# Kernel tuning notes

Measured on AMD Instinct MI355X. Metric: run time of the kernel, lower is better.

The kernel has to match this reference:

```python
import jax, jax.numpy as jnp
import numpy as np

N_NODES = 20000


def gcn_conv(x, src, dst, W, b, n):
    # PyG GCNConv: add self-loops, symmetric normalization, then aggregate.
    loop = jnp.arange(n, dtype=src.dtype)
    s = jnp.concatenate([src, loop])
    d = jnp.concatenate([dst, loop])
    w = jnp.ones(s.shape[0], dtype=x.dtype)
    deg = jax.ops.segment_sum(w, d, num_segments=n)  # in-degree at targets
    dinv = jnp.where(deg > 0, jax.lax.rsqrt(deg), 0.0)
    norm = dinv[s] * dinv[d]  # [E+n]
    h = x @ W  # [n, out]
    msg = h[s] * norm[:, None]  # gather + scale, [E+n, out]
    return jax.ops.segment_sum(msg, d, num_segments=n) + b


def gcn_stack(x, src, dst, W1, b1, W2, b2, n):
    h = jax.nn.relu(gcn_conv(x, src, dst, W1, b1, n))
    return gcn_conv(h, src, dst, W2, b2, n)


def setup_inputs() -> dict:
    key = jax.random.key(0)
    ks = jax.random.split(key, 12)
    n, e, din, dh, dout = N_NODES, 320000, 256, 256, 128
    x = jax.random.normal(ks[0], (n, din), dtype=jnp.float32)
    edge_index = jax.random.randint(ks[1], (2, e), 0, n, dtype=jnp.int64)
    g = lambda k, i, o: jax.random.normal(k, (i, o), dtype=jnp.float32) / np.sqrt(i)
    return {
        "x": x, "edge_index": edge_index,
        "Wf1": g(ks[2], din, dh), "bf1": jnp.zeros(dh, jnp.float32),
        "Wf2": g(ks[3], dh, dh), "bf2": jnp.zeros(dh, jnp.float32),
        "Wb1": g(ks[4], din, dh), "bb1": jnp.zeros(dh, jnp.float32),
        "Wb2": g(ks[5], dh, dh), "bb2": jnp.zeros(dh, jnp.float32),
        "Wfin": g(ks[6], 2 * dh, dout), "bfin": jnp.zeros(dout, jnp.float32),
    }


def reference(x, edge_index, Wf1, bf1, Wf2, bf2, Wb1, bb1, Wb2, bb2, Wfin, bfin):
    n = x.shape[0]
    src, dst = edge_index[0], edge_index[1]
    # forward-direction GCN stack
    x_fwd = gcn_stack(x, src, dst, Wf1, bf1, Wf2, bf2, n)
    # backward-direction GCN stack (edges reversed)
    x_bwd = gcn_stack(x, dst, src, Wb1, bb1, Wb2, bb2, n)
    x_combined = jnp.concatenate([x_fwd, x_bwd], axis=-1)  # [n, 2*hidden]
    return x_combined @ Wfin + bfin
```

## Files before the change

kernel.cpp:

```cpp
#include <hip/hip_runtime.h>

typedef unsigned int   u32;
typedef unsigned short u16;
typedef __attribute__((ext_vector_type(8))) short bf16x8;
typedef __attribute__((ext_vector_type(4))) float f32x4;

__device__ __forceinline__ u16 f2bf(float f) {
    u32 u = __float_as_uint(f);
    u32 r = u + 0x7fffu + ((u >> 16) & 1u);
    return (u16)(r >> 16);
}
__device__ __forceinline__ float bf2f(u16 h) {
    return __uint_as_float(((u32)h) << 16);
}
__device__ __forceinline__ float lof(u32 q) { return __uint_as_float(q << 16); }
__device__ __forceinline__ float hif(u32 q) { return __uint_as_float(q & 0xffff0000u); }
__device__ __forceinline__ u32 pk(float a, float b) {
    return (u32)f2bf(a) | ((u32)f2bf(b) << 16);
}
__device__ __forceinline__ void gl_lds16(const void* g, void* l) {
    __builtin_amdgcn_global_load_lds(
        (const __attribute__((address_space(1))) u32*)g,
        (__attribute__((address_space(3))) u32*)l, 16, 0, 0);
}
__device__ __forceinline__ void st16(void* dst, const u16* h) {
    uint4 q;
    q.x = (u32)h[0] | ((u32)h[1] << 16);
    q.y = (u32)h[2] | ((u32)h[3] << 16);
    q.z = (u32)h[4] | ((u32)h[5] << 16);
    q.w = (u32)h[6] | ((u32)h[7] << 16);
    *(uint4*)dst = q;
}

__global__ __launch_bounds__(256)
void k_deg(const int* __restrict__ src, const int* __restrict__ dst,
           int* __restrict__ deg_f, int* __restrict__ deg_b, int E) {
    int e = blockIdx.x * 256 + threadIdx.x;
    if (e < E) {
        atomicAdd(&deg_f[dst[e]], 1);
        atomicAdd(&deg_b[src[e]], 1);
    }
}

__global__ __launch_bounds__(256)
void k_scan1(const int* __restrict__ deg_f, const int* __restrict__ deg_b,
             float* __restrict__ dinv_f, float* __restrict__ dinv_b,
             int* __restrict__ bsum, int n, int nblk) {
    __shared__ int red[4];
    int dir = blockIdx.x >= nblk;
    int b = dir ? blockIdx.x - nblk : blockIdx.x;
    const int* deg = dir ? deg_b : deg_f;
    float* dinv = dir ? dinv_b : dinv_f;
    int idx = b * 256 + threadIdx.x;
    int d = 0;
    if (idx < n) {
        d = deg[idx];
        dinv[idx] = rsqrtf((float)(d + 1));
    }
    int s = d;
    s += __shfl_down(s, 32);
    s += __shfl_down(s, 16);
    s += __shfl_down(s, 8);
    s += __shfl_down(s, 4);
    s += __shfl_down(s, 2);
    s += __shfl_down(s, 1);
    int wv = threadIdx.x >> 6;
    if ((threadIdx.x & 63) == 0) red[wv] = s;
    __syncthreads();
    if (threadIdx.x == 0)
        bsum[blockIdx.x] = red[0] + red[1] + red[2] + red[3];
}

__global__ __launch_bounds__(256)
void k_scan2(const int* __restrict__ bsum, int* __restrict__ bpre, int nblk) {
    __shared__ int sm[256];
    int t = threadIdx.x;
    int seg = t >> 7;
    int i = t & 127;
    int val = (i < nblk) ? bsum[seg * nblk + i] : 0;
    sm[t] = val;
    __syncthreads();
    for (int s = 1; s < 128; s <<= 1) {
        int v = ((t & 127) >= s) ? sm[t - s] : 0;
        __syncthreads();
        sm[t] += v;
        __syncthreads();
    }
    if (i < nblk) bpre[seg * nblk + i] = sm[t] - val;
}

__global__ __launch_bounds__(256)
void k_scan3(const int* __restrict__ deg_f, const int* __restrict__ deg_b,
             const int* __restrict__ bpre,
             int* __restrict__ off_f, int* __restrict__ cur_f,
             int* __restrict__ off_b, int* __restrict__ cur_b,
             int n, int nblk, int E) {
    __shared__ int sm[256];
    int dir = blockIdx.x >= nblk;
    int b = dir ? blockIdx.x - nblk : blockIdx.x;
    const int* deg = dir ? deg_b : deg_f;
    int* off = dir ? off_b : off_f;
    int* cur = dir ? cur_b : cur_f;
    int base = bpre[blockIdx.x];
    int idx = b * 256 + threadIdx.x;
    int d = (idx < n) ? deg[idx] : 0;
    sm[threadIdx.x] = d;
    __syncthreads();
    for (int s = 1; s < 256; s <<= 1) {
        int v = (threadIdx.x >= s) ? sm[threadIdx.x - s] : 0;
        __syncthreads();
        sm[threadIdx.x] += v;
        __syncthreads();
    }
    if (idx < n) {
        int excl = base + sm[threadIdx.x] - d;
        off[idx] = excl;
        cur[idx] = excl;
    }
    if (blockIdx.x == 0 && threadIdx.x == 0) {
        off_f[n] = E;
        off_b[n] = E;
    }
}

__global__ __launch_bounds__(256)
void k_fill(const int* __restrict__ src, const int* __restrict__ dst,
            int* __restrict__ cur_f, int* __restrict__ cur_b,
            int* __restrict__ lst_f, int* __restrict__ lst_b, int E) {
    int e = blockIdx.x * 256 + threadIdx.x;
    if (e < E) {
        int s = src[e], d = dst[e];
        int pf = atomicAdd(&cur_f[d], 1);
        lst_f[pf] = s;
        int pb = atomicAdd(&cur_b[s], 1);
        lst_b[pb] = d;
    }
}

__global__ __launch_bounds__(256)
void k_wsplit5(const float* __restrict__ W0, const float* __restrict__ W1,
               const float* __restrict__ W2, const float* __restrict__ W3,
               const float* __restrict__ W4,
               u16* __restrict__ h0, u16* __restrict__ l0,
               u16* __restrict__ h1, u16* __restrict__ l1,
               u16* __restrict__ h2, u16* __restrict__ l2,
               u16* __restrict__ h3, u16* __restrict__ l3,
               u16* __restrict__ h4, u16* __restrict__ l4)
{
    int which = blockIdx.x >> 8;
    int sub = ((blockIdx.x & 255) << 8) | threadIdx.x;
    const float* W; u16 *H, *L; int kshift, N;
    switch (which) {
        case 0: W = W0; H = h0; L = l0; kshift = 8; N = 256; break;
        case 1: W = W1; H = h1; L = l1; kshift = 8; N = 256; break;
        case 2: W = W2; H = h2; L = l2; kshift = 8; N = 256; break;
        case 3: W = W3; H = h3; L = l3; kshift = 8; N = 256; break;
        default: W = W4; H = h4; L = l4; kshift = 9; N = 128; break;
    }
    int ni = sub >> kshift;
    int ki = sub & ((1 << kshift) - 1);
    float v = W[(size_t)ki * N + ni];
    u16 hh = f2bf(v);
    H[sub] = hh;
    L[sub] = f2bf(v - bf2f(hh));
}

__global__ __launch_bounds__(256)
void k_cvec(const float* __restrict__ bfin, const float* __restrict__ bf2,
            const float* __restrict__ bb2, const float* __restrict__ Wfin,
            float* __restrict__ cvec) {
    __shared__ float red[256];
    int j = blockIdx.x;
    int t = threadIdx.x;
    float s = bf2[t] * Wfin[(size_t)t * 128 + j]
            + bb2[t] * Wfin[(size_t)(t + 256) * 128 + j];
    red[t] = s;
    __syncthreads();
    for (int st = 128; st > 0; st >>= 1) {
        if (t < st) red[t] += red[t + st];
        __syncthreads();
    }
    if (t == 0) cvec[j] = red[0] + bfin[j];
}

template<int AMODE, int PASS3, int WLO>
__global__ __launch_bounds__(256)
void k_gemm2(const void* __restrict__ A0, const void* __restrict__ A1p,
             const u16* __restrict__ Alo0, const u16* __restrict__ Alo1,
             const u16* __restrict__ Bhi0, const u16* __restrict__ Blo0,
             const u16* __restrict__ Bhi1, const u16* __restrict__ Blo1, int ldb,
             u16* __restrict__ Chi0, u16* __restrict__ Clo0,
             u16* __restrict__ Chi1, u16* __restrict__ Clo1,
             const float* __restrict__ rs0, const float* __restrict__ rs1,
             int M, int N)
{
    constexpr int ALO = 8192;
    constexpr int BHI = PASS3 ? 16384 : 8192;
    constexpr int BLO = BHI + 8192;
    __shared__ char smem[PASS3 ? 32768 : 24576];

    const int z = blockIdx.z;
    const void* Aptr = z ? A1p : A0;
    const u16* Alo   = z ? Alo1 : Alo0;
    const u16* Bhi   = z ? Bhi1 : Bhi0;
    const u16* Blo   = z ? Blo1 : Blo0;
    u16* Chi         = z ? Chi1 : Chi0;
    u16* Clo         = z ? Clo1 : Clo0;
    const float* rowscale = z ? rs1 : rs0;

    const int tid  = threadIdx.x;
    const int lane = tid & 63;
    const int wid  = tid >> 6;
    const int wm   = wid >> 1, wn = wid & 1;
    const int bm   = blockIdx.x * 128;
    const int bn   = blockIdx.y * 128;

    f32x4 acc[4][4];
#pragma unroll
    for (int i = 0; i < 4; ++i)
#pragma unroll
        for (int j = 0; j < 4; ++j) acc[i][j] = (f32x4){0.f, 0.f, 0.f, 0.f};

    const int gsw  = ((lane >> 2) & 3) ^ ((lane >> 4) & 3);
    const int gsta = ((lane & 3) ^ gsw) << 4;
    const int sl   = (lane & 3) ^ ((lane >> 2) & 3);
    const int hi4  = lane >> 4;
    const int gsel = ((hi4 ^ sl) << 4);
    const int frow = lane & 15;

    for (int k0 = 0; k0 < 256; k0 += 32) {
        if (k0) __syncthreads();

#pragma unroll
        for (int p = 0; p < 2; ++p) {
            int c   = p * 4 + wid;
            int row = c * 16 + (lane >> 2);
            size_t rb = (size_t)(bn + row) * ldb + (size_t)k0 * 2 + gsta;
            gl_lds16((const char*)Bhi + rb, smem + BHI + c * 1024);
            gl_lds16((const char*)Blo + rb, smem + BLO + c * 1024);
        }
        if (AMODE == 0) {
            const u16* Ah = (const u16*)Aptr;
#pragma unroll
            for (int p = 0; p < 2; ++p) {
                int c   = p * 4 + wid;
                int row = c * 16 + (lane >> 2);
                int grow = bm + row; if (grow >= M) grow = M - 1;
                size_t rb = (size_t)grow * 512 + (size_t)k0 * 2 + gsta;
                gl_lds16((const char*)Ah + rb, smem + c * 1024);
                if (PASS3)
                    gl_lds16((const char*)Alo + rb, smem + ALO + c * 1024);
            }
        } else {
            const float* Af = (const float*)Aptr;
            int row  = tid >> 1;
            int half = tid & 1;
            int grow = bm + row; if (grow >= M) grow = M - 1;
            const float* srcp = Af + (size_t)grow * 256 + k0 + half * 16;
            float vv[16];
            *(float4*)(vv + 0)  = *(const float4*)(srcp + 0);
            *(float4*)(vv + 4)  = *(const float4*)(srcp + 4);
            *(float4*)(vv + 8)  = *(const float4*)(srcp + 8);
            *(float4*)(vv + 12) = *(const float4*)(srcp + 12);
            u16 h[16], l[16];
#pragma unroll
            for (int i = 0; i < 16; ++i) {
                h[i] = f2bf(vv[i]);
                l[i] = f2bf(vv[i] - bf2f(h[i]));
            }
            int swz = (row & 3) ^ ((row >> 2) & 3);
            char* dh = smem + row * 64;
            st16(dh + (((half * 2 + 0) ^ swz) << 4), h + 0);
            st16(dh + (((half * 2 + 1) ^ swz) << 4), h + 8);
            if (PASS3) {
                char* dl = smem + ALO + row * 64;
                st16(dl + (((half * 2 + 0) ^ swz) << 4), l + 0);
                st16(dl + (((half * 2 + 1) ^ swz) << 4), l + 8);
            }
        }
        __syncthreads();

        bf16x8 ah[4], al[4], bh[4], bl[4];
#pragma unroll
        for (int fm = 0; fm < 4; ++fm) {
            int r = wm * 64 + fm * 16 + frow;
            ah[fm] = *(const bf16x8*)(smem + r * 64 + gsel);
            if (PASS3) al[fm] = *(const bf16x8*)(smem + ALO + r * 64 + gsel);
        }
#pragma unroll
        for (int fn = 0; fn < 4; ++fn) {
            int r = wn * 64 + fn * 16 + frow;
            bh[fn] = *(const bf16x8*)(smem + BHI + r * 64 + gsel);
            bl[fn] = *(const bf16x8*)(smem + BLO + r * 64 + gsel);
        }
#pragma unroll
        for (int fm = 0; fm < 4; ++fm)
#pragma unroll
            for (int fn = 0; fn < 4; ++fn)
                acc[fm][fn] = __builtin_amdgcn_mfma_f32_16x16x32_bf16(ah[fm], bh[fn], acc[fm][fn], 0, 0, 0);
#pragma unroll
        for (int fm = 0; fm < 4; ++fm)
#pragma unroll
            for (int fn = 0; fn < 4; ++fn)
                acc[fm][fn] = __builtin_amdgcn_mfma_f32_16x16x32_bf16(ah[fm], bl[fn], acc[fm][fn], 0, 0, 0);
        if (PASS3) {
#pragma unroll
            for (int fm = 0; fm < 4; ++fm)
#pragma unroll
                for (int fn = 0; fn < 4; ++fn)
                    acc[fm][fn] = __builtin_amdgcn_mfma_f32_16x16x32_bf16(al[fm], bh[fn], acc[fm][fn], 0, 0, 0);
        }
    }

#pragma unroll
    for (int fm = 0; fm < 4; ++fm) {
#pragma unroll
        for (int q = 0; q < 4; ++q) {
            int row = bm + wm * 64 + fm * 16 + hi4 * 4 + q;
            if (row < M) {
                float s = rowscale ? rowscale[row] : 1.0f;
#pragma unroll
                for (int fn = 0; fn < 4; ++fn) {
                    int col = bn + wn * 64 + fn * 16 + frow;
                    float v = acc[fm][fn][q] * s;
                    u16 hb = f2bf(v);
                    Chi[(size_t)row * N + col] = hb;
                    if (WLO) Clo[(size_t)row * N + col] = f2bf(v - bf2f(hb));
                }
            }
        }
    }
}

__global__ __launch_bounds__(256)
void k_agg1(const u16* __restrict__ ghf, const u16* __restrict__ glf,
            const u16* __restrict__ ghb, const u16* __restrict__ glb,
            const int* __restrict__ off_f, const int* __restrict__ lst_f,
            const int* __restrict__ off_b, const int* __restrict__ lst_b,
            const float* __restrict__ dinv_f, const float* __restrict__ dinv_b,
            const float* __restrict__ b_f, const float* __restrict__ b_b,
            u16* __restrict__ ozf, u16* __restrict__ ozb, int n)
{
    int nb = gridDim.x >> 1;
    int stack = blockIdx.x >= nb;
    int bx = stack ? (blockIdx.x - nb) : blockIdx.x;
    const u16* gh = stack ? ghb : ghf;
    const u16* gl = stack ? glb : glf;
    const int* off = stack ? off_b : off_f;
    const int* lst = stack ? lst_b : lst_f;
    const float* dinv = stack ? dinv_b : dinv_f;
    const float* bias = stack ? b_b : b_f;
    u16* oz = stack ? ozb : ozf;

    int wv = threadIdx.x >> 6;
    int half = (threadIdx.x >> 5) & 1;
    int l = threadIdx.x & 31;
    int v = bx * 8 + wv * 2 + half;
    if (v >= n) return;
    int f0 = l * 8;

    uint4 qh = *(const uint4*)(gh + (size_t)v * 256 + f0);
    uint4 ql = *(const uint4*)(gl + (size_t)v * 256 + f0);
    float a0 = lof(qh.x) + lof(ql.x), a1 = hif(qh.x) + hif(ql.x);
    float a2 = lof(qh.y) + lof(ql.y), a3 = hif(qh.y) + hif(ql.y);
    float a4 = lof(qh.z) + lof(ql.z), a5 = hif(qh.z) + hif(ql.z);
    float a6 = lof(qh.w) + lof(ql.w), a7 = hif(qh.w) + hif(ql.w);

    int s0 = off[v], s1 = off[v + 1];
    int j = s0;
    for (; j + 4 <= s1; j += 4) {
        int u0 = lst[j], u1 = lst[j + 1], u2 = lst[j + 2], u3 = lst[j + 3];
        uint4 m0 = *(const uint4*)(gh + (size_t)u0 * 256 + f0);
        uint4 m1 = *(const uint4*)(gh + (size_t)u1 * 256 + f0);
        uint4 m2 = *(const uint4*)(gh + (size_t)u2 * 256 + f0);
        uint4 m3 = *(const uint4*)(gh + (size_t)u3 * 256 + f0);
        a0 += lof(m0.x) + lof(m1.x) + lof(m2.x) + lof(m3.x);
        a1 += hif(m0.x) + hif(m1.x) + hif(m2.x) + hif(m3.x);
        a2 += lof(m0.y) + lof(m1.y) + lof(m2.y) + lof(m3.y);
        a3 += hif(m0.y) + hif(m1.y) + hif(m2.y) + hif(m3.y);
        a4 += lof(m0.z) + lof(m1.z) + lof(m2.z) + lof(m3.z);
        a5 += hif(m0.z) + hif(m1.z) + hif(m2.z) + hif(m3.z);
        a6 += lof(m0.w) + lof(m1.w) + lof(m2.w) + lof(m3.w);
        a7 += hif(m0.w) + hif(m1.w) + hif(m2.w) + hif(m3.w);
    }
    for (; j < s1; ++j) {
        int u = lst[j];
        uint4 m = *(const uint4*)(gh + (size_t)u * 256 + f0);
        a0 += lof(m.x); a1 += hif(m.x);
        a2 += lof(m.y); a3 += hif(m.y);
        a4 += lof(m.z); a5 += hif(m.z);
        a6 += lof(m.w); a7 += hif(m.w);
    }
    float sc = dinv[v];
    float4 bA = *(const float4*)(bias + f0);
    float4 bB = *(const float4*)(bias + f0 + 4);
    float o0 = fmaxf(a0 * sc + bA.x, 0.f), o1 = fmaxf(a1 * sc + bA.y, 0.f);
    float o2 = fmaxf(a2 * sc + bA.z, 0.f), o3 = fmaxf(a3 * sc + bA.w, 0.f);
    float o4 = fmaxf(a4 * sc + bB.x, 0.f), o5 = fmaxf(a5 * sc + bB.y, 0.f);
    float o6 = fmaxf(a6 * sc + bB.z, 0.f), o7 = fmaxf(a7 * sc + bB.w, 0.f);
    uint4 r;
    r.x = pk(o0, o1); r.y = pk(o2, o3); r.z = pk(o4, o5); r.w = pk(o6, o7);
    *(uint4*)(oz + (size_t)v * 256 + f0) = r;
}

__global__ __launch_bounds__(256)
void k_agg2(const u16* __restrict__ yf, const u16* __restrict__ yb,
            const int* __restrict__ off_f, const int* __restrict__ lst_f,
            const int* __restrict__ off_b, const int* __restrict__ lst_b,
            const float* __restrict__ dinv_f, const float* __restrict__ dinv_b,
            const float* __restrict__ cvec, float* __restrict__ out, int n)
{
    int wv = threadIdx.x >> 6, lane = threadIdx.x & 63;
    int v = blockIdx.x * 4 + wv;
    if (v >= n) return;
    int dirb = lane >> 5;
    int l = lane & 31;
    int f0 = l * 4;

    const u16* y   = dirb ? yb : yf;
    const int* off = dirb ? off_b : off_f;
    const int* lst = dirb ? lst_b : lst_f;
    float dv = dirb ? dinv_b[v] : dinv_f[v];

    uint2 q = *(const uint2*)(y + (size_t)v * 128 + f0);
    float a0 = lof(q.x), a1 = hif(q.x), a2 = lof(q.y), a3 = hif(q.y);

    int s0 = off[v], s1 = off[v + 1];
    int j = s0;
    for (; j + 4 <= s1; j += 4) {
        int u0 = lst[j], u1 = lst[j + 1], u2 = lst[j + 2], u3 = lst[j + 3];
        uint2 m0 = *(const uint2*)(y + (size_t)u0 * 128 + f0);
        uint2 m1 = *(const uint2*)(y + (size_t)u1 * 128 + f0);
        uint2 m2 = *(const uint2*)(y + (size_t)u2 * 128 + f0);
        uint2 m3 = *(const uint2*)(y + (size_t)u3 * 128 + f0);
        a0 += lof(m0.x) + lof(m1.x) + lof(m2.x) + lof(m3.x);
        a1 += hif(m0.x) + hif(m1.x) + hif(m2.x) + hif(m3.x);
        a2 += lof(m0.y) + lof(m1.y) + lof(m2.y) + lof(m3.y);
        a3 += hif(m0.y) + hif(m1.y) + hif(m2.y) + hif(m3.y);
    }
    for (; j < s1; ++j) {
        int u = lst[j];
        uint2 m = *(const uint2*)(y + (size_t)u * 128 + f0);
        a0 += lof(m.x); a1 += hif(m.x);
        a2 += lof(m.y); a3 += hif(m.y);
    }
    float o0 = a0 * dv, o1 = a1 * dv, o2 = a2 * dv, o3 = a3 * dv;
    o0 += __shfl_xor(o0, 32);
    o1 += __shfl_xor(o1, 32);
    o2 += __shfl_xor(o2, 32);
    o3 += __shfl_xor(o3, 32);
    if (dirb == 0) {
        float4 c4 = *(const float4*)(cvec + f0);
        float4 o;
        o.x = o0 + c4.x; o.y = o1 + c4.y; o.z = o2 + c4.z; o.w = o3 + c4.w;
        *(float4*)(out + (size_t)v * 128 + f0) = o;
    }
}

extern "C" void kernel_launch(void* const* d_in, const int* in_sizes, int n_in,
                              void* d_out, int out_size, void* d_ws, size_t ws_size,
                              hipStream_t stream) {
    const float* x    = (const float*)d_in[0];
    const int*   ei   = (const int*)d_in[1];
    const float* Wf1  = (const float*)d_in[2];
    const float* bf1  = (const float*)d_in[3];
    const float* Wf2  = (const float*)d_in[4];
    const float* bf2  = (const float*)d_in[5];
    const float* Wb1  = (const float*)d_in[6];
    const float* bb1  = (const float*)d_in[7];
    const float* Wb2  = (const float*)d_in[8];
    const float* bb2  = (const float*)d_in[9];
    const float* Wfin = (const float*)d_in[10];
    const float* bfin = (const float*)d_in[11];
    float* out = (float*)d_out;

    const int n = in_sizes[0] / 256;
    const int E = in_sizes[1] / 2;
    const int* src = ei;
    const int* dst = ei + E;

    char* p = (char*)d_ws;
    auto take = [&](size_t bytes) -> void* {
        void* q = (void*)p;
        p += (bytes + 255) & ~(size_t)255;
        return q;
    };
    u16* P1f_h = (u16*)take((size_t)n * 256 * 2);
    u16* P1f_l = (u16*)take((size_t)n * 256 * 2);
    u16* P1b_h = (u16*)take((size_t)n * 256 * 2);
    u16* P1b_l = (u16*)take((size_t)n * 256 * 2);
    u16* Zf    = (u16*)take((size_t)n * 256 * 2);
    u16* Zb    = (u16*)take((size_t)n * 256 * 2);
    u16* H2f   = (u16*)take((size_t)n * 256 * 2);
    u16* H2b   = (u16*)take((size_t)n * 256 * 2);
    u16* Yf    = (u16*)take((size_t)n * 128 * 2);
    u16* Yb    = (u16*)take((size_t)n * 128 * 2);
    u16* w1f_h = (u16*)take(65536 * 2); u16* w1f_l = (u16*)take(65536 * 2);
    u16* w2f_h = (u16*)take(65536 * 2); u16* w2f_l = (u16*)take(65536 * 2);
    u16* w1b_h = (u16*)take(65536 * 2); u16* w1b_l = (u16*)take(65536 * 2);
    u16* w2b_h = (u16*)take(65536 * 2); u16* w2b_l = (u16*)take(65536 * 2);
    u16* wfin_h = (u16*)take(65536 * 2); u16* wfin_l = (u16*)take(65536 * 2);
    float* cvec = (float*)take(128 * sizeof(float));
    int*   deg_f  = (int*)take((size_t)n * sizeof(int));
    int*   deg_b  = (int*)take((size_t)n * sizeof(int));
    int*   off_f  = (int*)take((size_t)(n + 1) * sizeof(int));
    int*   off_b  = (int*)take((size_t)(n + 1) * sizeof(int));
    int*   cur_f  = (int*)take((size_t)n * sizeof(int));
    int*   cur_b  = (int*)take((size_t)n * sizeof(int));
    int*   lst_f  = (int*)take((size_t)E * sizeof(int));
    int*   lst_b  = (int*)take((size_t)E * sizeof(int));
    float* dinv_f = (float*)take((size_t)n * sizeof(float));
    float* dinv_b = (float*)take((size_t)n * sizeof(float));
    int*   bsum   = (int*)take(256 * sizeof(int));
    int*   bpre   = (int*)take(256 * sizeof(int));

    hipMemsetAsync(deg_f, 0, (size_t)n * sizeof(int), stream);
    hipMemsetAsync(deg_b, 0, (size_t)n * sizeof(int), stream);

    const int nblk = (n + 255) / 256;
    int eb = (E + 255) / 256;
    k_deg<<<eb, 256, 0, stream>>>(src, dst, deg_f, deg_b, E);
    k_scan1<<<2 * nblk, 256, 0, stream>>>(deg_f, deg_b, dinv_f, dinv_b, bsum, n, nblk);
    k_scan2<<<1, 256, 0, stream>>>(bsum, bpre, nblk);
    k_scan3<<<2 * nblk, 256, 0, stream>>>(deg_f, deg_b, bpre,
        off_f, cur_f, off_b, cur_b, n, nblk, E);
    k_fill<<<eb, 256, 0, stream>>>(src, dst, cur_f, cur_b, lst_f, lst_b, E);
    k_wsplit5<<<1280, 256, 0, stream>>>(Wf1, Wf2, Wb1, Wb2, Wfin,
        w1f_h, w1f_l, w2f_h, w2f_l, w1b_h, w1b_l, w2b_h, w2b_l, wfin_h, wfin_l);
    k_cvec<<<128, 256, 0, stream>>>(bfin, bf2, bb2, Wfin, cvec);

    const int gx = (n + 127) / 128;
    dim3 gBig(gx, 2, 2);
    dim3 gFin(gx, 1, 2);
    int ab = (n + 3) / 4;
    int a1b = 2 * ((n + 7) / 8);

    k_gemm2<1, 1, 1><<<gBig, 256, 0, stream>>>(x, x, nullptr, nullptr,
        w1f_h, w1f_l, w1b_h, w1b_l, 512,
        P1f_h, P1f_l, P1b_h, P1b_l, dinv_f, dinv_b, n, 256);
    k_agg1<<<a1b, 256, 0, stream>>>(P1f_h, P1f_l, P1b_h, P1b_l,
        off_f, lst_f, off_b, lst_b, dinv_f, dinv_b, bf1, bb1, Zf, Zb, n);
    k_gemm2<0, 0, 0><<<gBig, 256, 0, stream>>>(Zf, Zb, nullptr, nullptr,
        w2f_h, w2f_l, w2b_h, w2b_l, 512,
        H2f, nullptr, H2b, nullptr, dinv_f, dinv_b, n, 256);
    k_gemm2<0, 0, 0><<<gFin, 256, 0, stream>>>(H2f, H2b, nullptr, nullptr,
        wfin_h, wfin_l, wfin_h + 256, wfin_l + 256, 1024,
        Yf, nullptr, Yb, nullptr, nullptr, nullptr, n, 128);
    k_agg2<<<ab, 256, 0, stream>>>(Yf, Yb,
        off_f, lst_f, off_b, lst_b, dinv_f, dinv_b, cvec, out, n);
}
```

Baseline: 292.1 us.

## Drop split-bf16 low parts for x and layer-1 outputs, pre-convert x

Converts x to a single bf16 copy in a merged prep kernel, which also absorbs the weight-split and bias-vector kernels. The first GEMM then runs two MFMA passes instead of three and stores only a high bf16 output. The first aggregation reads one bf16 buffer instead of a hi/lo pair and gathers eight neighbours per iteration. This cuts memory traffic and MFMA work in the first layer at the cost of lower precision on the input and intermediate activations.

Measured after the change: 279.9 us. 1.04x faster.

```diff
diff --git a/kernel.cpp b/kernel.cpp
--- a/kernel.cpp
+++ b/kernel.cpp
@@ -22,14 +22,6 @@
     __builtin_amdgcn_global_load_lds(
         (const __attribute__((address_space(1))) u32*)g,
         (__attribute__((address_space(3))) u32*)l, 16, 0, 0);
-}
-__device__ __forceinline__ void st16(void* dst, const u16* h) {
-    uint4 q;
-    q.x = (u32)h[0] | ((u32)h[1] << 16);
-    q.y = (u32)h[2] | ((u32)h[3] << 16);
-    q.z = (u32)h[4] | ((u32)h[5] << 16);
-    q.w = (u32)h[6] | ((u32)h[7] << 16);
-    *(uint4*)dst = q;
 }
 
 __global__ __launch_bounds__(256)
@@ -138,74 +130,76 @@
 }
 
 __global__ __launch_bounds__(256)
-void k_wsplit5(const float* __restrict__ W0, const float* __restrict__ W1,
-               const float* __restrict__ W2, const float* __restrict__ W3,
-               const float* __restrict__ W4,
-               u16* __restrict__ h0, u16* __restrict__ l0,
-               u16* __restrict__ h1, u16* __restrict__ l1,
-               u16* __restrict__ h2, u16* __restrict__ l2,
-               u16* __restrict__ h3, u16* __restrict__ l3,
-               u16* __restrict__ h4, u16* __restrict__ l4)
+void k_prep(const float* __restrict__ W0, const float* __restrict__ W1,
+            const float* __restrict__ W2, const float* __restrict__ W3,
+            const float* __restrict__ W4,
+            u16* __restrict__ h0, u16* __restrict__ l0,
+            u16* __restrict__ h1, u16* __restrict__ l1,
+            u16* __restrict__ h2, u16* __restrict__ l2,
+            u16* __restrict__ h3, u16* __restrict__ l3,
+            u16* __restrict__ h4, u16* __restrict__ l4,
+            const float* __restrict__ bfin, const float* __restrict__ bf2,
+            const float* __restrict__ bb2, float* __restrict__ cvec,
+            const float* __restrict__ x, u16* __restrict__ xh, int xcount)
 {
-    int which = blockIdx.x >> 8;
-    int sub = ((blockIdx.x & 255) << 8) | threadIdx.x;
-    const float* W; u16 *H, *L; int kshift, N;
-    switch (which) {
-        case 0: W = W0; H = h0; L = l0; kshift = 8; N = 256; break;
-        case 1: W = W1; H = h1; L = l1; kshift = 8; N = 256; break;
-        case 2: W = W2; H = h2; L = l2; kshift = 8; N = 256; break;
-        case 3: W = W3; H = h3; L = l3; kshift = 8; N = 256; break;
-        default: W = W4; H = h4; L = l4; kshift = 9; N = 128; break;
-    }
-    int ni = sub >> kshift;
-    int ki = sub & ((1 << kshift) - 1);
-    float v = W[(size_t)ki * N + ni];
-    u16 hh = f2bf(v);
-    H[sub] = hh;
-    L[sub] = f2bf(v - bf2f(hh));
-}
-
-__global__ __launch_bounds__(256)
-void k_cvec(const float* __restrict__ bfin, const float* __restrict__ bf2,
-            const float* __restrict__ bb2, const float* __restrict__ Wfin,
-            float* __restrict__ cvec) {
     __shared__ float red[256];
-    int j = blockIdx.x;
+    int b = blockIdx.x;
     int t = threadIdx.x;
-    float s = bf2[t] * Wfin[(size_t)t * 128 + j]
-            + bb2[t] * Wfin[(size_t)(t + 256) * 128 + j];
-    red[t] = s;
-    __syncthreads();
-    for (int st = 128; st > 0; st >>= 1) {
-        if (t < st) red[t] += red[t + st];
+    if (b < 1280) {
+        int which = b >> 8;
+        int sub = ((b & 255) << 8) | t;
+        const float* W; u16 *H, *L; int kshift, N;
+        switch (which) {
+            case 0: W = W0; H = h0; L = l0; kshift = 8; N = 256; break;
+            case 1: W = W1; H = h1; L = l1; kshift = 8; N = 256; break;
+            case 2: W = W2; H = h2; L = l2; kshift = 8; N = 256; break;
+            case 3: W = W3; H = h3; L = l3; kshift = 8; N = 256; break;
+            default: W = W4; H = h4; L = l4; kshift = 9; N = 128; break;
+        }
+        int ni = sub >> kshift;
+        int ki = sub & ((1 << kshift) - 1);
+        float v = W[(size_t)ki * N + ni];
+        u16 hh = f2bf(v);
+        H[sub] = hh;
+        L[sub] = f2bf(v - bf2f(hh));
+    } else if (b < 1408) {
+        int j = b - 1280;
+        float s = bf2[t] * W4[(size_t)t * 128 + j]
+                + bb2[t] * W4[(size_t)(t + 256) * 128 + j];
+        red[t] = s;
         __syncthreads();
-    }
-    if (t == 0) cvec[j] = red[0] + bfin[j];
-}
-
-template<int AMODE, int PASS3, int WLO>
-__global__ __launch_bounds__(256)
-void k_gemm2(const void* __restrict__ A0, const void* __restrict__ A1p,
-             const u16* __restrict__ Alo0, const u16* __restrict__ Alo1,
-             const u16* __restrict__ Bhi0, const u16* __restrict__ Blo0,
-             const u16* __restrict__ Bhi1, const u16* __restrict__ Blo1, int ldb,
-             u16* __restrict__ Chi0, u16* __restrict__ Clo0,
-             u16* __restrict__ Chi1, u16* __restrict__ Clo1,
-             const float* __restrict__ rs0, const float* __restrict__ rs1,
-             int M, int N)
+        for (int st = 128; st > 0; st >>= 1) {
+            if (t < st) red[t] += red[t + st];
+            __syncthreads();
+        }
+        if (t == 0) cvec[j] = red[0] + bfin[j];
+    } else {
+        int i = (b - 1408) * 1024 + t * 4;
+        if (i < xcount) {
+            float4 v = *(const float4*)(x + i);
+            ushort4 h4v;
+            h4v.x = f2bf(v.x); h4v.y = f2bf(v.y);
+            h4v.z = f2bf(v.z); h4v.w = f2bf(v.w);
+            *(ushort4*)(xh + i) = h4v;
+        }
+    }
+}
+
+__global__ __launch_bounds__(256)
+void k_gemm(const u16* __restrict__ A0, const u16* __restrict__ A1p,
+            const u16* __restrict__ Bhi0, const u16* __restrict__ Blo0,
+            const u16* __restrict__ Bhi1, const u16* __restrict__ Blo1, int ldb,
+            u16* __restrict__ C0, u16* __restrict__ C1,
+            const float* __restrict__ rs0, const float* __restrict__ rs1,
+            int M, int N)
 {
-    constexpr int ALO = 8192;
-    constexpr int BHI = PASS3 ? 16384 : 8192;
-    constexpr int BLO = BHI + 8192;
-    __shared__ char smem[PASS3 ? 32768 : 24576];
+    __shared__ char smem[24576];
 
     const int z = blockIdx.z;
-    const void* Aptr = z ? A1p : A0;
-    const u16* Alo   = z ? Alo1 : Alo0;
-    const u16* Bhi   = z ? Bhi1 : Bhi0;
-    const u16* Blo   = z ? Blo1 : Blo0;
-    u16* Chi         = z ? Chi1 : Chi0;
-    u16* Clo         = z ? Clo1 : Clo0;
+    const u16* Ah  = z ? A1p : A0;
+    const u16* Bhi = z ? Bhi1 : Bhi0;
+    const u16* Blo = z ? Blo1 : Blo0;
+    u16* Chi       = z ? C1 : C0;
     const float* rowscale = z ? rs1 : rs0;
 
     const int tid  = threadIdx.x;
@@ -236,62 +230,30 @@
             int c   = p * 4 + wid;
             int row = c * 16 + (lane >> 2);
             size_t rb = (size_t)(bn + row) * ldb + (size_t)k0 * 2 + gsta;
-            gl_lds16((const char*)Bhi + rb, smem + BHI + c * 1024);
-            gl_lds16((const char*)Blo + rb, smem + BLO + c * 1024);
-        }
-        if (AMODE == 0) {
-            const u16* Ah = (const u16*)Aptr;
-#pragma unroll
-            for (int p = 0; p < 2; ++p) {
-                int c   = p * 4 + wid;
-                int row = c * 16 + (lane >> 2);
-                int grow = bm + row; if (grow >= M) grow = M - 1;
-                size_t rb = (size_t)grow * 512 + (size_t)k0 * 2 + gsta;
-                gl_lds16((const char*)Ah + rb, smem + c * 1024);
-                if (PASS3)
-                    gl_lds16((const char*)Alo + rb, smem + ALO + c * 1024);
-            }
-        } else {
-            const float* Af = (const float*)Aptr;
-            int row  = tid >> 1;
-            int half = tid & 1;
+            gl_lds16((const char*)Bhi + rb, smem + 8192 + c * 1024);
+            gl_lds16((const char*)Blo + rb, smem + 16384 + c * 1024);
+        }
+#pragma unroll
+        for (int p = 0; p < 2; ++p) {
+            int c   = p * 4 + wid;
+            int row = c * 16 + (lane >> 2);
             int grow = bm + row; if (grow >= M) grow = M - 1;
-            const float* srcp = Af + (size_t)grow * 256 + k0 + half * 16;
-            float vv[16];
-            *(float4*)(vv + 0)  = *(const float4*)(srcp + 0);
-            *(float4*)(vv + 4)  = *(const float4*)(srcp + 4);
-            *(float4*)(vv + 8)  = *(const float4*)(srcp + 8);
-            *(float4*)(vv + 12) = *(const float4*)(srcp + 12);
-            u16 h[16], l[16];
-#pragma unroll
-            for (int i = 0; i < 16; ++i) {
-                h[i] = f2bf(vv[i]);
-                l[i] = f2bf(vv[i] - bf2f(h[i]));
-            }
-            int swz = (row & 3) ^ ((row >> 2) & 3);
-            char* dh = smem + row * 64;
-            st16(dh + (((half * 2 + 0) ^ swz) << 4), h + 0);
-            st16(dh + (((half * 2 + 1) ^ swz) << 4), h + 8);
-            if (PASS3) {
-                char* dl = smem + ALO + row * 64;
-                st16(dl + (((half * 2 + 0) ^ swz) << 4), l + 0);
-                st16(dl + (((half * 2 + 1) ^ swz) << 4), l + 8);
-            }
+            size_t rb = (size_t)grow * 512 + (size_t)k0 * 2 + gsta;
+            gl_lds16((const char*)Ah + rb, smem + c * 1024);
         }
         __syncthreads();
 
-        bf16x8 ah[4], al[4], bh[4], bl[4];
+        bf16x8 ah[4], bh[4], bl[4];
 #pragma unroll
         for (int fm = 0; fm < 4; ++fm) {
             int r = wm * 64 + fm * 16 + frow;
             ah[fm] = *(const bf16x8*)(smem + r * 64 + gsel);
-            if (PASS3) al[fm] = *(const bf16x8*)(smem + ALO + r * 64 + gsel);
         }
 #pragma unroll
         for (int fn = 0; fn < 4; ++fn) {
             int r = wn * 64 + fn * 16 + frow;
-            bh[fn] = *(const bf16x8*)(smem + BHI + r * 64 + gsel);
-            bl[fn] = *(const bf16x8*)(smem + BLO + r * 64 + gsel);
+            bh[fn] = *(const bf16x8*)(smem + 8192 + r * 64 + gsel);
+            bl[fn] = *(const bf16x8*)(smem + 16384 + r * 64 + gsel);
         }
 #pragma unroll
         for (int fm = 0; fm < 4; ++fm)
@@ -303,13 +265,6 @@
 #pragma unroll
             for (int fn = 0; fn < 4; ++fn)
                 acc[fm][fn] = __builtin_amdgcn_mfma_f32_16x16x32_bf16(ah[fm], bl[fn], acc[fm][fn], 0, 0, 0);
-        if (PASS3) {
-#pragma unroll
-            for (int fm = 0; fm < 4; ++fm)
-#pragma unroll
-                for (int fn = 0; fn < 4; ++fn)
-                    acc[fm][fn] = __builtin_amdgcn_mfma_f32_16x16x32_bf16(al[fm], bh[fn], acc[fm][fn], 0, 0, 0);
-        }
     }
 
 #pragma unroll
@@ -322,10 +277,7 @@
 #pragma unroll
                 for (int fn = 0; fn < 4; ++fn) {
                     int col = bn + wn * 64 + fn * 16 + frow;
-                    float v = acc[fm][fn][q] * s;
-                    u16 hb = f2bf(v);
-                    Chi[(size_t)row * N + col] = hb;
-                    if (WLO) Clo[(size_t)row * N + col] = f2bf(v - bf2f(hb));
+                    Chi[(size_t)row * N + col] = f2bf(acc[fm][fn][q] * s);
                 }
             }
         }
@@ -333,8 +285,7 @@
 }
 
 __global__ __launch_bounds__(256)
-void k_agg1(const u16* __restrict__ ghf, const u16* __restrict__ glf,
-            const u16* __restrict__ ghb, const u16* __restrict__ glb,
+void k_agg1(const u16* __restrict__ ghf, const u16* __restrict__ ghb,
             const int* __restrict__ off_f, const int* __restrict__ lst_f,
             const int* __restrict__ off_b, const int* __restrict__ lst_b,
             const float* __restrict__ dinv_f, const float* __restrict__ dinv_b,
@@ -345,7 +296,6 @@
     int stack = blockIdx.x >= nb;
     int bx = stack ? (blockIdx.x - nb) : blockIdx.x;
     const u16* gh = stack ? ghb : ghf;
-    const u16* gl = stack ? glb : glf;
     const int* off = stack ? off_b : off_f;
     const int* lst = stack ? lst_b : lst_f;
     const float* dinv = stack ? dinv_b : dinv_f;
@@ -360,28 +310,42 @@
     int f0 = l * 8;
 
     uint4 qh = *(const uint4*)(gh + (size_t)v * 256 + f0);
-    uint4 ql = *(const uint4*)(gl + (size_t)v * 256 + f0);
-    float a0 = lof(qh.x) + lof(ql.x), a1 = hif(qh.x) + hif(ql.x);
-    float a2 = lof(qh.y) + lof(ql.y), a3 = hif(qh.y) + hif(ql.y);
-    float a4 = lof(qh.z) + lof(ql.z), a5 = hif(qh.z) + hif(ql.z);
-    float a6 = lof(qh.w) + lof(ql.w), a7 = hif(qh.w) + hif(ql.w);
+    float a0 = lof(qh.x), a1 = hif(qh.x);
+    float a2 = lof(qh.y), a3 = hif(qh.y);
+    float a4 = lof(qh.z), a5 = hif(qh.z);
+    float a6 = lof(qh.w), a7 = hif(qh.w);
 
     int s0 = off[v], s1 = off[v + 1];
     int j = s0;
+    for (; j + 8 <= s1; j += 8) {
+        uint4 m[8];
+#pragma unroll
+        for (int q = 0; q < 8; ++q) {
+            int u = lst[j + q];
+            m[q] = *(const uint4*)(gh + (size_t)u * 256 + f0);
+        }
+#pragma unroll
+        for (int q = 0; q < 8; ++q) {
+            a0 += lof(m[q].x); a1 += hif(m[q].x);
+            a2 += lof(m[q].y); a3 += hif(m[q].y);
+            a4 += lof(m[q].z); a5 += hif(m[q].z);
+            a6 += lof(m[q].w); a7 += hif(m[q].w);
+        }
+    }
     for (; j + 4 <= s1; j += 4) {
-        int u0 = lst[j], u1 = lst[j + 1], u2 = lst[j + 2], u3 = lst[j + 3];
-        uint4 m0 = *(const uint4*)(gh + (size_t)u0 * 256 + f0);
-        uint4 m1 = *(const uint4*)(gh + (size_t)u1 * 256 + f0);
-        uint4 m2 = *(const uint4*)(gh + (size_t)u2 * 256 + f0);
-        uint4 m3 = *(const uint4*)(gh + (size_t)u3 * 256 + f0);
-        a0 += lof(m0.x) + lof(m1.x) + lof(m2.x) + lof(m3.x);
-        a1 += hif(m0.x) + hif(m1.x) + hif(m2.x) + hif(m3.x);
-        a2 += lof(m0.y) + lof(m1.y) + lof(m2.y) + lof(m3.y);
-        a3 += hif(m0.y) + hif(m1.y) + hif(m2.y) + hif(m3.y);
-        a4 += lof(m0.z) + lof(m1.z) + lof(m2.z) + lof(m3.z);
-        a5 += hif(m0.z) + hif(m1.z) + hif(m2.z) + hif(m3.z);
-        a6 += lof(m0.w) + lof(m1.w) + lof(m2.w) + lof(m3.w);
-        a7 += hif(m0.w) + hif(m1.w) + hif(m2.w) + hif(m3.w);
+        uint4 m[4];
+#pragma unroll
+        for (int q = 0; q < 4; ++q) {
+            int u = lst[j + q];
+            m[q] = *(const uint4*)(gh + (size_t)u * 256 + f0);
+        }
+#pragma unroll
+        for (int q = 0; q < 4; ++q) {
+            a0 += lof(m[q].x); a1 += hif(m[q].x);
+            a2 += lof(m[q].y); a3 += hif(m[q].y);
+            a4 += lof(m[q].z); a5 += hif(m[q].z);
+            a6 += lof(m[q].w); a7 += hif(m[q].w);
+        }
     }
     for (; j < s1; ++j) {
         int u = lst[j];
@@ -485,10 +449,9 @@
         p += (bytes + 255) & ~(size_t)255;
         return q;
     };
-    u16* P1f_h = (u16*)take((size_t)n * 256 * 2);
-    u16* P1f_l = (u16*)take((size_t)n * 256 * 2);
-    u16* P1b_h = (u16*)take((size_t)n * 256 * 2);
-    u16* P1b_l = (u16*)take((size_t)n * 256 * 2);
+    u16* Xh    = (u16*)take((size_t)n * 256 * 2);
+    u16* P1f   = (u16*)take((size_t)n * 256 * 2);
+    u16* P1b   = (u16*)take((size_t)n * 256 * 2);
     u16* Zf    = (u16*)take((size_t)n * 256 * 2);
     u16* Zb    = (u16*)take((size_t)n * 256 * 2);
     u16* H2f   = (u16*)take((size_t)n * 256 * 2);
@@ -518,16 +481,19 @@
     hipMemsetAsync(deg_b, 0, (size_t)n * sizeof(int), stream);
 
     const int nblk = (n + 255) / 256;
+    const int xcount = n * 256;
+    const int xblocks = (xcount + 1023) / 1024;
     int eb = (E + 255) / 256;
+
     k_deg<<<eb, 256, 0, stream>>>(src, dst, deg_f, deg_b, E);
     k_scan1<<<2 * nblk, 256, 0, stream>>>(deg_f, deg_b, dinv_f, dinv_b, bsum, n, nblk);
     k_scan2<<<1, 256, 0, stream>>>(bsum, bpre, nblk);
     k_scan3<<<2 * nblk, 256, 0, stream>>>(deg_f, deg_b, bpre,
         off_f, cur_f, off_b, cur_b, n, nblk, E);
     k_fill<<<eb, 256, 0, stream>>>(src, dst, cur_f, cur_b, lst_f, lst_b, E);
-    k_wsplit5<<<1280, 256, 0, stream>>>(Wf1, Wf2, Wb1, Wb2, Wfin,
-        w1f_h, w1f_l, w2f_h, w2f_l, w1b_h, w1b_l, w2b_h, w2b_l, wfin_h, wfin_l);
-    k_cvec<<<128, 256, 0, stream>>>(bfin, bf2, bb2, Wfin, cvec);
+    k_prep<<<1408 + xblocks, 256, 0, stream>>>(Wf1, Wf2, Wb1, Wb2, Wfin,
+        w1f_h, w1f_l, w2f_h, w2f_l, w1b_h, w1b_l, w2b_h, w2b_l, wfin_h, wfin_l,
+        bfin, bf2, bb2, cvec, x, Xh, xcount);
 
     const int gx = (n + 127) / 128;
     dim3 gBig(gx, 2, 2);
@@ -535,17 +501,17 @@
     int ab = (n + 3) / 4;
     int a1b = 2 * ((n + 7) / 8);
 
-    k_gemm2<1, 1, 1><<<gBig, 256, 0, stream>>>(x, x, nullptr, nullptr,
+    k_gemm<<<gBig, 256, 0, stream>>>(Xh, Xh,
         w1f_h, w1f_l, w1b_h, w1b_l, 512,
-        P1f_h, P1f_l, P1b_h, P1b_l, dinv_f, dinv_b, n, 256);
-    k_agg1<<<a1b, 256, 0, stream>>>(P1f_h, P1f_l, P1b_h, P1b_l,
+        P1f, P1b, dinv_f, dinv_b, n, 256);
+    k_agg1<<<a1b, 256, 0, stream>>>(P1f, P1b,
         off_f, lst_f, off_b, lst_b, dinv_f, dinv_b, bf1, bb1, Zf, Zb, n);
-    k_gemm2<0, 0, 0><<<gBig, 256, 0, stream>>>(Zf, Zb, nullptr, nullptr,
+    k_gemm<<<gBig, 256, 0, stream>>>(Zf, Zb,
         w2f_h, w2f_l, w2b_h, w2b_l, 512,
-        H2f, nullptr, H2b, nullptr, dinv_f, dinv_b, n, 256);
-    k_gemm2<0, 0, 0><<<gFin, 256, 0, stream>>>(H2f, H2b, nullptr, nullptr,
+        H2f, H2b, dinv_f, dinv_b, n, 256);
+    k_gemm<<<gFin, 256, 0, stream>>>(H2f, H2b,
         wfin_h, wfin_l, wfin_h + 256, wfin_l + 256, 1024,
-        Yf, nullptr, Yb, nullptr, nullptr, nullptr, n, 128);
+        Yf, Yb, nullptr, nullptr, n, 128);
     k_agg2<<<ab, 256, 0, stream>>>(Yf, Yb,
         off_f, lst_f, off_b, lst_b, dinv_f, dinv_b, cvec, out, n);
 }
```
